# Performance work log

Measured on AMD Instinct MI355X. Metric: run time of the kernel, lower is better.

Reference implementation:

```python
import jax, jax.numpy as jnp
import numpy as np

B = 256          # batch of images
TOK = 256        # 16x16 tokens per image
V = 1024         # codebook size
D = 256          # code dim


def setup_inputs() -> dict:
    key = jax.random.key(0)
    k1, k2, k3, k4 = jax.random.split(key, 4)
    image_seq = jax.random.randint(k1, (B, TOK), 0, V, dtype=jnp.int64)
    image_seq2 = jax.random.randint(k2, (B, TOK), 0, V, dtype=jnp.int64)
    alpha = jax.random.uniform(k3, (1,), dtype=jnp.float32)
    W = jax.random.normal(k4, (V, D), dtype=jnp.float32)
    return {"image_seq": image_seq, "image_seq2": image_seq2, "alpha": alpha, "W": W}


def reference(image_seq, image_seq2, alpha, W):
    a = alpha[0]
    # gather codebook entries: [B, TOK, D]
    emb = W[image_seq]
    emb2 = W[image_seq2]
    x = (1.0 - a) * emb + a * emb2
    xf = x.reshape(-1, D)                        # [N, D], N = B*TOK
    # brute-force L2 distance to every code, without materializing [N, V, D]:
    d = (jnp.sum(xf * xf, axis=-1, keepdims=True)
         - 2.0 * xf @ W.T
         + jnp.sum(W * W, axis=-1)[None, :])
    idx = jnp.argmin(d, axis=1)                  # top-1 nearest code, [N]
    # get_codebook_entry: gather, reshape to bhwc, permute to bchw
    z_q = W[idx].reshape(B, 16, 16, D)           # [B, 16, 16, 256]
    z_q = jnp.transpose(z_q, (0, 3, 1, 2))       # [B, 256, 16, 16]
    return z_q
```

## Files before the change

### kernel.cpp

```cpp
#include <hip/hip_runtime.h>

static constexpr int Vn = 1024;
static constexpr int Dn = 256;
static constexpr int NT = 65536;

typedef float vfloat4 __attribute__((ext_vector_type(4)));

__global__ __launch_bounds__(256) void gram_kernel(const float* __restrict__ W,
                                                   float* __restrict__ G,
                                                   float* __restrict__ norms) {
    __shared__ float As[32][68];
    __shared__ float Bs[32][36];
    const int tid = threadIdx.x;
    const int tx = tid & 7;
    const int ty = tid >> 3;
    const int bm = blockIdx.y * 64;
    const int bn = blockIdx.x * 32;
    const float4* Wv = (const float4*)W;

    const int m0  = tid >> 3;
    const int kql = tid & 7;

    float4 pa[2], pb;
#pragma unroll
    for (int s = 0; s < 2; ++s)
        pa[s] = Wv[(bm + m0 + 32 * s) * 64 + kql];
    pb = Wv[(bn + m0) * 64 + kql];

    float acc[2][4] = {};
    for (int c = 0; c < 8; ++c) {
#pragma unroll
        for (int s = 0; s < 2; ++s) {
            const int m = m0 + 32 * s;
            As[kql * 4 + 0][m] = pa[s].x;
            As[kql * 4 + 1][m] = pa[s].y;
            As[kql * 4 + 2][m] = pa[s].z;
            As[kql * 4 + 3][m] = pa[s].w;
        }
        Bs[kql * 4 + 0][m0] = pb.x;
        Bs[kql * 4 + 1][m0] = pb.y;
        Bs[kql * 4 + 2][m0] = pb.z;
        Bs[kql * 4 + 3][m0] = pb.w;
        __syncthreads();
        if (c < 7) {
            const int kq = (c + 1) * 8 + kql;
#pragma unroll
            for (int s = 0; s < 2; ++s)
                pa[s] = Wv[(bm + m0 + 32 * s) * 64 + kq];
            pb = Wv[(bn + m0) * 64 + kq];
        }
        const float* Ab = &As[0][ty * 2];
        const float* Bb = &Bs[0][tx * 4];
        float2 a_c = *(const float2*)Ab;
        float4 b_c = *(const float4*)Bb;
#pragma unroll
        for (int kk = 0; kk < 32; ++kk) {
            const int kn = (kk < 31) ? kk + 1 : kk;
            const float2 a_n = *(const float2*)(Ab + kn * 68);
            const float4 b_n = *(const float4*)(Bb + kn * 36);
            const float a_s[2] = {a_c.x, a_c.y};
            const float b_s[4] = {b_c.x, b_c.y, b_c.z, b_c.w};
#pragma unroll
            for (int u = 0; u < 2; ++u)
#pragma unroll
                for (int w = 0; w < 4; ++w)
                    acc[u][w] = fmaf(a_s[u], b_s[w], acc[u][w]);
            a_c = a_n;
            b_c = b_n;
        }
        __syncthreads();
    }
#pragma unroll
    for (int u = 0; u < 2; ++u) {
        const int row = bm + ty * 2 + u;
        vfloat4 o;
        o.x = acc[u][0]; o.y = acc[u][1]; o.z = acc[u][2]; o.w = acc[u][3];
        __builtin_nontemporal_store(o, (vfloat4*)(G + row * Vn + bn + tx * 4));
        const int cd = row - (bn + tx * 4);
        if (cd >= 0 && cd < 4) norms[row] = acc[u][cd];
    }
}

__global__ __launch_bounds__(256) void argmin_kernel(const int* __restrict__ seq,
                                                     const int* __restrict__ seq2,
                                                     const float* __restrict__ alpha,
                                                     const float* __restrict__ G,
                                                     const float* __restrict__ norms,
                                                     int* __restrict__ bestV) {
    const int tid  = threadIdx.x;
    const int wave = tid >> 6;
    const int lane = tid & 63;
    const int t0   = blockIdx.x * 32;

    float4 nn_r[4];
#pragma unroll
    for (int s = 0; s < 4; ++s) nn_r[s] = ((const float4*)norms)[s * 64 + lane];

    const float a  = alpha[0];
    const float c0 = -2.0f * (1.0f - a);
    const float c1 = -2.0f * a;

    for (int bb = 0; bb < 2; ++bb) {
        const int base_t = t0 + wave * 8 + bb * 4;
        int iv[4], jv[4];
#pragma unroll
        for (int q = 0; q < 4; ++q) { iv[q] = seq[base_t + q]; jv[q] = seq2[base_t + q]; }
#pragma unroll
        for (int pair = 0; pair < 2; ++pair) {
            const int qa = pair * 2, qb = pair * 2 + 1;
            const float4* GiA = (const float4*)(G + iv[qa] * Vn);
            const float4* GjA = (const float4*)(G + jv[qa] * Vn);
            const float4* GiB = (const float4*)(G + iv[qb] * Vn);
            const float4* GjB = (const float4*)(G + jv[qb] * Vn);
            float4 gia[4], gja[4], gib[4], gjb[4];
#pragma unroll
            for (int s = 0; s < 4; ++s) {
                const int e = s * 64 + lane;
                gia[s] = GiA[e];
                gja[s] = GjA[e];
                gib[s] = GiB[e];
                gjb[s] = GjB[e];
            }
            float bestA = __builtin_inff(), bestB = __builtin_inff();
            int vA = 0, vB = 0;
#pragma unroll
            for (int s = 0; s < 4; ++s) {
                const int e = s * 64 + lane;
                const float4 nn = nn_r[s];
                const int v = e * 4;
                {
                    const float s0 = fmaf(c1, gja[s].x, fmaf(c0, gia[s].x, nn.x));
                    const float s1 = fmaf(c1, gja[s].y, fmaf(c0, gia[s].y, nn.y));
                    const float s2 = fmaf(c1, gja[s].z, fmaf(c0, gia[s].z, nn.z));
                    const float s3 = fmaf(c1, gja[s].w, fmaf(c0, gia[s].w, nn.w));
                    if (s0 < bestA) { bestA = s0; vA = v; }
                    if (s1 < bestA) { bestA = s1; vA = v + 1; }
                    if (s2 < bestA) { bestA = s2; vA = v + 2; }
                    if (s3 < bestA) { bestA = s3; vA = v + 3; }
                }
                {
                    const float s0 = fmaf(c1, gjb[s].x, fmaf(c0, gib[s].x, nn.x));
                    const float s1 = fmaf(c1, gjb[s].y, fmaf(c0, gib[s].y, nn.y));
                    const float s2 = fmaf(c1, gjb[s].z, fmaf(c0, gib[s].z, nn.z));
                    const float s3 = fmaf(c1, gjb[s].w, fmaf(c0, gib[s].w, nn.w));
                    if (s0 < bestB) { bestB = s0; vB = v; }
                    if (s1 < bestB) { bestB = s1; vB = v + 1; }
                    if (s2 < bestB) { bestB = s2; vB = v + 2; }
                    if (s3 < bestB) { bestB = s3; vB = v + 3; }
                }
            }
#pragma unroll
            for (int off = 32; off >= 1; off >>= 1) {
                const float oa = __shfl_down(bestA, off, 64);
                const int   va = __shfl_down(vA, off, 64);
                if (oa < bestA || (oa == bestA && va < vA)) { bestA = oa; vA = va; }
                const float ob = __shfl_down(bestB, off, 64);
                const int   vb = __shfl_down(vB, off, 64);
                if (ob < bestB || (ob == bestB && vb < vB)) { bestB = ob; vB = vb; }
            }
            if (lane == 0) {
                bestV[base_t + qa] = vA;
                bestV[base_t + qb] = vB;
            }
        }
    }
}

__global__ __launch_bounds__(256) void write_kernel(const int* __restrict__ bestV,
                                                    const float* __restrict__ W,
                                                    float* __restrict__ out) {
    __shared__ float T[32][129];
    const int tid = threadIdx.x;
    const int t0  = blockIdx.x * 32;
    const int b   = t0 >> 8;
    const int hw0 = t0 & 255;
    float* outb = out + b * 65536 + hw0;
    const int tok  = tid >> 3;
    const int l8   = tid & 7;
    const int hw4  = (tid & 7) * 4;
    const int drow = tid >> 3;
    const int v = bestV[t0 + tok];
#pragma unroll
    for (int half = 0; half < 2; ++half) {
        const float4* Wr = (const float4*)(W + v * Dn + half * 128);
#pragma unroll
        for (int p = 0; p < 4; ++p) {
            const int d4 = p * 8 + l8;
            const float4 w4 = Wr[d4];
            T[tok][d4 * 4 + 0] = w4.x;
            T[tok][d4 * 4 + 1] = w4.y;
            T[tok][d4 * 4 + 2] = w4.z;
            T[tok][d4 * 4 + 3] = w4.w;
        }
        __syncthreads();
#pragma unroll
        for (int dp = 0; dp < 128; dp += 32) {
            const int dl = dp + drow;
            const int d = half * 128 + dl;
            vfloat4 o;
            o.x = T[hw4 + 0][dl];
            o.y = T[hw4 + 1][dl];
            o.z = T[hw4 + 2][dl];
            o.w = T[hw4 + 3][dl];
            __builtin_nontemporal_store(o, (vfloat4*)(outb + d * 256 + hw4));
        }
        __syncthreads();
    }
}

extern "C" void kernel_launch(void* const* d_in, const int* in_sizes, int n_in,
                              void* d_out, int out_size, void* d_ws, size_t ws_size,
                              hipStream_t stream) {
    const int*   seq   = (const int*)d_in[0];
    const int*   seq2  = (const int*)d_in[1];
    const float* alpha = (const float*)d_in[2];
    const float* W     = (const float*)d_in[3];
    float* out = (float*)d_out;

    char* ws = (char*)d_ws;
    float* G     = (float*)(ws);
    float* norms = (float*)(ws + 4194304);
    int*   bestV = (int*)(ws + 4194304 + 4096);

    gram_kernel<<<dim3(32, 16), 256, 0, stream>>>(W, G, norms);
    argmin_kernel<<<NT / 32, 256, 0, stream>>>(seq, seq2, alpha, G, norms, bestV);
    write_kernel<<<NT / 32, 256, 0, stream>>>(bestV, W, out);
}
```

Before: 128.4 us.

## Exploit Gram matrix symmetry by computing only upper-triangular tiles

Replaces the full 1024x1024 Gram GEMM with a kernel that computes only the 528 upper-triangle 32x32 tiles and mirrors each off-diagonal tile into the transposed location. Diagonal blocks write the code norms. The kernel also moves to 64-thread blocks with a 4x4 per-thread microtile. This roughly halves the FLOPs of the gram stage, at the cost of smaller blocks, a serial loop to decode the tile index, and strided transposed stores.

```diff
diff --git a/kernel.cpp b/kernel.cpp
--- a/kernel.cpp
+++ b/kernel.cpp
@@ -6,62 +6,68 @@
 
 typedef float vfloat4 __attribute__((ext_vector_type(4)));
 
-__global__ __launch_bounds__(256) void gram_kernel(const float* __restrict__ W,
-                                                   float* __restrict__ G,
-                                                   float* __restrict__ norms) {
-    __shared__ float As[32][68];
+__global__ __launch_bounds__(64) void gram_sym_kernel(const float* __restrict__ W,
+                                                      float* __restrict__ G,
+                                                      float* __restrict__ norms) {
+    __shared__ float As[32][36];
     __shared__ float Bs[32][36];
     const int tid = threadIdx.x;
-    const int tx = tid & 7;
-    const int ty = tid >> 3;
-    const int bm = blockIdx.y * 64;
-    const int bn = blockIdx.x * 32;
+
+    int L = blockIdx.x, ti = 0;
+    while (L >= 32 - ti) { L -= 32 - ti; ++ti; }
+    const int tj = ti + L;
+    const int bm = ti * 32;
+    const int bn = tj * 32;
     const float4* Wv = (const float4*)W;
 
     const int m0  = tid >> 3;
     const int kql = tid & 7;
-
-    float4 pa[2], pb;
-#pragma unroll
-    for (int s = 0; s < 2; ++s)
-        pa[s] = Wv[(bm + m0 + 32 * s) * 64 + kql];
-    pb = Wv[(bn + m0) * 64 + kql];
-
-    float acc[2][4] = {};
+    const int tx  = tid & 7;
+    const int ty  = tid >> 3;
+
+    float4 pa[4], pb[4];
+#pragma unroll
+    for (int s = 0; s < 4; ++s) {
+        pa[s] = Wv[(bm + m0 + 8 * s) * 64 + kql];
+        pb[s] = Wv[(bn + m0 + 8 * s) * 64 + kql];
+    }
+
+    float acc[4][4] = {};
     for (int c = 0; c < 8; ++c) {
 #pragma unroll
-        for (int s = 0; s < 2; ++s) {
-            const int m = m0 + 32 * s;
+        for (int s = 0; s < 4; ++s) {
+            const int m = m0 + 8 * s;
             As[kql * 4 + 0][m] = pa[s].x;
             As[kql * 4 + 1][m] = pa[s].y;
             As[kql * 4 + 2][m] = pa[s].z;
             As[kql * 4 + 3][m] = pa[s].w;
-        }
-        Bs[kql * 4 + 0][m0] = pb.x;
-        Bs[kql * 4 + 1][m0] = pb.y;
-        Bs[kql * 4 + 2][m0] = pb.z;
-        Bs[kql * 4 + 3][m0] = pb.w;
+            Bs[kql * 4 + 0][m] = pb[s].x;
+            Bs[kql * 4 + 1][m] = pb[s].y;
+            Bs[kql * 4 + 2][m] = pb[s].z;
+            Bs[kql * 4 + 3][m] = pb[s].w;
+        }
         __syncthreads();
         if (c < 7) {
             const int kq = (c + 1) * 8 + kql;
 #pragma unroll
-            for (int s = 0; s < 2; ++s)
-                pa[s] = Wv[(bm + m0 + 32 * s) * 64 + kq];
-            pb = Wv[(bn + m0) * 64 + kq];
-        }
-        const float* Ab = &As[0][ty * 2];
+            for (int s = 0; s < 4; ++s) {
+                pa[s] = Wv[(bm + m0 + 8 * s) * 64 + kq];
+                pb[s] = Wv[(bn + m0 + 8 * s) * 64 + kq];
+            }
+        }
+        const float* Ab = &As[0][ty * 4];
         const float* Bb = &Bs[0][tx * 4];
-        float2 a_c = *(const float2*)Ab;
+        float4 a_c = *(const float4*)Ab;
         float4 b_c = *(const float4*)Bb;
 #pragma unroll
         for (int kk = 0; kk < 32; ++kk) {
             const int kn = (kk < 31) ? kk + 1 : kk;
-            const float2 a_n = *(const float2*)(Ab + kn * 68);
+            const float4 a_n = *(const float4*)(Ab + kn * 36);
             const float4 b_n = *(const float4*)(Bb + kn * 36);
-            const float a_s[2] = {a_c.x, a_c.y};
+            const float a_s[4] = {a_c.x, a_c.y, a_c.z, a_c.w};
             const float b_s[4] = {b_c.x, b_c.y, b_c.z, b_c.w};
 #pragma unroll
-            for (int u = 0; u < 2; ++u)
+            for (int u = 0; u < 4; ++u)
 #pragma unroll
                 for (int w = 0; w < 4; ++w)
                     acc[u][w] = fmaf(a_s[u], b_s[w], acc[u][w]);
@@ -71,13 +77,23 @@
         __syncthreads();
     }
 #pragma unroll
-    for (int u = 0; u < 2; ++u) {
-        const int row = bm + ty * 2 + u;
+    for (int u = 0; u < 4; ++u) {
+        const int row = bm + ty * 4 + u;
         vfloat4 o;
         o.x = acc[u][0]; o.y = acc[u][1]; o.z = acc[u][2]; o.w = acc[u][3];
         __builtin_nontemporal_store(o, (vfloat4*)(G + row * Vn + bn + tx * 4));
-        const int cd = row - (bn + tx * 4);
-        if (cd >= 0 && cd < 4) norms[row] = acc[u][cd];
+    }
+    if (ti != tj) {
+#pragma unroll
+        for (int w = 0; w < 4; ++w) {
+            const int col = bn + tx * 4 + w;
+            vfloat4 o;
+            o.x = acc[0][w]; o.y = acc[1][w]; o.z = acc[2][w]; o.w = acc[3][w];
+            __builtin_nontemporal_store(o, (vfloat4*)(G + col * Vn + bm + ty * 4));
+        }
+    } else if (tx == ty) {
+#pragma unroll
+        for (int u = 0; u < 4; ++u) norms[bm + ty * 4 + u] = acc[u][u];
     }
 }
 
@@ -222,7 +238,7 @@
     float* norms = (float*)(ws + 4194304);
     int*   bestV = (int*)(ws + 4194304 + 4096);
 
-    gram_kernel<<<dim3(32, 16), 256, 0, stream>>>(W, G, norms);
+    gram_sym_kernel<<<528, 64, 0, stream>>>(W, G, norms);
     argmin_kernel<<<NT / 32, 256, 0, stream>>>(seq, seq2, alpha, G, norms, bestV);
     write_kernel<<<NT / 32, 256, 0, stream>>>(bestV, W, out);
 }
```

New measurement: 128.4 us. About the same (-0.0%).
